# Optimization experiments

Measured on AMD Instinct MI355X. Metric: run time of the kernel, lower is better.

Reference implementation:

```python
import jax, jax.numpy as jnp
import numpy as np

NUM_HEADS = 8
BN_EPS = 1e-5
ATTN_EPS = 1e-6

def setup_inputs() -> dict:
    key = jax.random.key(0)
    N, E, D = 50000, 600000, 128
    ks = jax.random.split(key, 7)
    s = 1.0 / np.sqrt(D).astype(np.float32)
    return {
        'x': jax.random.normal(ks[0], (N, D), jnp.float32),
        'edge_attr': jax.random.normal(ks[1], (E, D), jnp.float32),
        'WQ': jax.random.normal(ks[2], (D, D), jnp.float32) * s,
        'WK': jax.random.normal(ks[3], (D, D), jnp.float32) * s,
        'WV': jax.random.normal(ks[4], (D, D), jnp.float32) * s,
        'WE': jax.random.normal(ks[5], (D, D), jnp.float32) * s,
        'bn_gamma': jnp.ones((D,), jnp.float32),
        'bn_beta': jnp.zeros((D,), jnp.float32),
        'edge_index': jax.random.randint(ks[6], (2, E), 0, N, dtype=jnp.int32),
    }

def reference(x, edge_attr, WQ, WK, WV, WE, bn_gamma, bn_beta, edge_index):
    N, D = x.shape
    H = NUM_HEADS
    dh = D // H  # head dim
    # Projections (no bias), split into heads: [N, H, dh]
    Q = (x @ WQ).reshape(N, H, dh)
    K = (x @ WK).reshape(N, H, dh)
    V = (x @ WV).reshape(N, H, dh)
    Eh = (edge_attr @ WE).reshape(-1, H, dh)  # [E, H, dh]
    src, dst = edge_index[0], edge_index[1]
    # Per-edge attention score modulated by edge features
    score = (K[src] * Q[dst]) / jnp.sqrt(jnp.float32(dh)) * Eh  # [E, H, dh]
    score = jnp.exp(jnp.clip(score.sum(-1, keepdims=True), -5.0, 5.0))  # [E, H, 1]
    msg = V[src] * score  # [E, H, dh]
    wV = jax.ops.segment_sum(msg, dst, num_segments=N)  # [N, H, dh]
    Z = jax.ops.segment_sum(score, dst, num_segments=N)  # [N, H, 1]
    h_attn = (wV / (Z + ATTN_EPS)).reshape(N, D)
    # Residual (dropout p=0 is identity) + BatchNorm1d (training statistics)
    h = x + h_attn
    mean = h.mean(axis=0)
    var = jnp.mean((h - mean) ** 2, axis=0)
    return (h - mean) * jax.lax.rsqrt(var + BN_EPS) * bn_gamma + bn_beta
```

## Files before the change

kernel.cpp:

```cpp
#include <hip/hip_runtime.h>
#include <math.h>


typedef __attribute__((ext_vector_type(8))) short short8;
typedef __attribute__((ext_vector_type(4))) float f32x4;

__device__ __forceinline__ unsigned short f2bf(float x) {
    unsigned int u = __float_as_uint(x);
    return (unsigned short)((u + 0x7FFFu + ((u >> 16) & 1u)) >> 16);
}

__global__ __launch_bounds__(128) void qkv_kernel(
    const float* __restrict__ x, const float* __restrict__ WQ,
    const float* __restrict__ WK, const float* __restrict__ WV,
    float* __restrict__ Q, float* __restrict__ K, float* __restrict__ V,
    int N)
{
    const int t = threadIdx.x;
    const int r0 = blockIdx.x * 8;
    __shared__ float xs[8][128];
#pragma unroll
    for (int r = 0; r < 8; ++r)
        xs[r][t] = (r0 + r < N) ? x[(size_t)(r0 + r) * 128 + t] : 0.f;
    __syncthreads();

    float aq[8] = {0}, ak[8] = {0}, av[8] = {0};
#pragma unroll 2
    for (int k4 = 0; k4 < 32; ++k4) {
        const float* wq = WQ + (size_t)(k4 * 4) * 128 + t;
        const float* wk = WK + (size_t)(k4 * 4) * 128 + t;
        const float* wv = WV + (size_t)(k4 * 4) * 128 + t;
        float q0 = wq[0], q1 = wq[128], q2 = wq[256], q3 = wq[384];
        float k0 = wk[0], k1 = wk[128], k2 = wk[256], k3 = wk[384];
        float v0 = wv[0], v1 = wv[128], v2 = wv[256], v3 = wv[384];
#pragma unroll
        for (int r = 0; r < 8; ++r) {
            float4 xv = *(const float4*)&xs[r][k4 * 4];
            aq[r] += xv.x * q0 + xv.y * q1 + xv.z * q2 + xv.w * q3;
            ak[r] += xv.x * k0 + xv.y * k1 + xv.z * k2 + xv.w * k3;
            av[r] += xv.x * v0 + xv.y * v1 + xv.z * v2 + xv.w * v3;
        }
    }
#pragma unroll
    for (int r = 0; r < 8; ++r) {
        if (r0 + r < N) {
            const size_t o = (size_t)(r0 + r) * 128 + t;
            Q[o] = aq[r]; K[o] = ak[r]; V[o] = av[r];
        }
    }
}

__global__ __launch_bounds__(256) void wet_kernel(
    const float* __restrict__ WE, unsigned short* __restrict__ WEt)
{
    const int i = blockIdx.x * 256 + threadIdx.x;
    const int n = i >> 7, k = i & 127;
    WEt[i] = f2bf(WE[k * 128 + n]);
}

#define ASTRIDE 136
#define ESTRIDE 132

__global__ __launch_bounds__(256, 4) void eh_score_kernel(
    const float* __restrict__ ea, const unsigned short* __restrict__ WEt,
    const float* __restrict__ Q, const float* __restrict__ K,
    const int* __restrict__ src, const int* __restrict__ dst,
    float* __restrict__ score, int E)
{
    union Sm {
        unsigned short A[64 * ASTRIDE];
        float eh[64 * ESTRIDE];
    };
    __shared__ Sm sm;
    __shared__ int ssrc[64], sdst[64];
    const int t = threadIdx.x;
    const long e0 = (long)blockIdx.x * 64;

#pragma unroll
    for (int kk = 0; kk < 8; ++kk) {
        const int f = t + kk * 256;
        const int row = f >> 5, c4 = (f & 31) * 4;
        float4 v = make_float4(0.f, 0.f, 0.f, 0.f);
        if (e0 + row < E) v = *(const float4*)&ea[(size_t)(e0 + row) * 128 + c4];
        unsigned long long pk =  (unsigned long long)f2bf(v.x)
                              | ((unsigned long long)f2bf(v.y) << 16)
                              | ((unsigned long long)f2bf(v.z) << 32)
                              | ((unsigned long long)f2bf(v.w) << 48);
        *(unsigned long long*)&sm.A[row * ASTRIDE + c4] = pk;
    }
    if (t < 64) {
        const long e = e0 + t;
        ssrc[t] = (e < E) ? src[e] : 0;
        sdst[t] = (e < E) ? dst[e] : 0;
    }
    __syncthreads();

    const int w = t >> 6, l = t & 63;
    const int rb = (w >> 1) * 32, cb = (w & 1) * 64;
    const int lr = l & 15, quad = l >> 4;

    f32x4 acc[2][4];
#pragma unroll
    for (int i = 0; i < 2; ++i)
#pragma unroll
        for (int j = 0; j < 4; ++j) acc[i][j] = (f32x4){0.f, 0.f, 0.f, 0.f};

#pragma unroll
    for (int kb = 0; kb < 4; ++kb) {
        const int k0 = kb * 32 + quad * 8;
        short8 a0 = *(const short8*)&sm.A[(rb + lr) * ASTRIDE + k0];
        short8 a1 = *(const short8*)&sm.A[(rb + 16 + lr) * ASTRIDE + k0];
        short8 b0 = *(const short8*)&WEt[(cb + lr) * 128 + k0];
        short8 b1 = *(const short8*)&WEt[(cb + 16 + lr) * 128 + k0];
        short8 b2 = *(const short8*)&WEt[(cb + 32 + lr) * 128 + k0];
        short8 b3 = *(const short8*)&WEt[(cb + 48 + lr) * 128 + k0];
        acc[0][0] = __builtin_amdgcn_mfma_f32_16x16x32_bf16(a0, b0, acc[0][0], 0, 0, 0);
        acc[0][1] = __builtin_amdgcn_mfma_f32_16x16x32_bf16(a0, b1, acc[0][1], 0, 0, 0);
        acc[0][2] = __builtin_amdgcn_mfma_f32_16x16x32_bf16(a0, b2, acc[0][2], 0, 0, 0);
        acc[0][3] = __builtin_amdgcn_mfma_f32_16x16x32_bf16(a0, b3, acc[0][3], 0, 0, 0);
        acc[1][0] = __builtin_amdgcn_mfma_f32_16x16x32_bf16(a1, b0, acc[1][0], 0, 0, 0);
        acc[1][1] = __builtin_amdgcn_mfma_f32_16x16x32_bf16(a1, b1, acc[1][1], 0, 0, 0);
        acc[1][2] = __builtin_amdgcn_mfma_f32_16x16x32_bf16(a1, b2, acc[1][2], 0, 0, 0);
        acc[1][3] = __builtin_amdgcn_mfma_f32_16x16x32_bf16(a1, b3, acc[1][3], 0, 0, 0);
    }
    __syncthreads();

#pragma unroll
    for (int mi = 0; mi < 2; ++mi)
#pragma unroll
        for (int ni = 0; ni < 4; ++ni)
#pragma unroll
            for (int r = 0; r < 4; ++r)
                sm.eh[(rb + mi * 16 + quad * 4 + r) * ESTRIDE + cb + ni * 16 + lr] =
                    acc[mi][ni][r];
    __syncthreads();

#pragma unroll
    for (int pp = 0; pp < 2; ++pp) {
        const int p = t + pp * 256;
        const int e = p >> 3, h = p & 7;
        const long ge = e0 + e;
        if (ge < E) {
            const float* kp = K + (size_t)ssrc[e] * 128 + h * 16;
            const float* qp = Q + (size_t)sdst[e] * 128 + h * 16;
            const float* ep = &sm.eh[e * ESTRIDE + h * 16];
            float s = 0.f;
#pragma unroll
            for (int j = 0; j < 4; ++j) {
                float4 kv = *(const float4*)&kp[j * 4];
                float4 qv = *(const float4*)&qp[j * 4];
                float4 ev = *(const float4*)&ep[j * 4];
                s += kv.x * qv.x * ev.x + kv.y * qv.y * ev.y +
                     kv.z * qv.z * ev.z + kv.w * qv.w * ev.w;
            }
            score[ge * 8 + h] = __expf(fminf(fmaxf(s * 0.25f, -5.f), 5.f));
        }
    }
}

__global__ __launch_bounds__(256) void hist_kernel(
    const int* __restrict__ dst, int* __restrict__ counts, int E)
{
    const int e = blockIdx.x * 256 + threadIdx.x;
    if (e < E) atomicAdd(&counts[dst[e]], 1);
}

__global__ __launch_bounds__(256) void scan_chunk_kernel(
    const int* __restrict__ in, int* __restrict__ excl,
    int* __restrict__ chunksums, int n)
{
    __shared__ int sm[256];
    const int t = threadIdx.x;
    const int i = blockIdx.x * 256 + t;
    const int v = (i < n) ? in[i] : 0;
    sm[t] = v;
    __syncthreads();
#pragma unroll
    for (int off = 1; off < 256; off <<= 1) {
        const int a = (t >= off) ? sm[t - off] : 0;
        __syncthreads();
        sm[t] += a;
        __syncthreads();
    }
    if (i < n) excl[i] = sm[t] - v;
    if (t == 255 && chunksums) chunksums[blockIdx.x] = sm[255];
}

__global__ __launch_bounds__(256) void add_offsets_kernel(
    int* __restrict__ excl, int* __restrict__ cursor,
    const int* __restrict__ chunkoff, int n)
{
    const int i = blockIdx.x * 256 + threadIdx.x;
    if (i < n) {
        const int v = excl[i] + chunkoff[blockIdx.x];
        excl[i] = v;
        cursor[i] = v;
    }
}

__global__ __launch_bounds__(256) void fill_perm_kernel(
    const int* __restrict__ dst, int* __restrict__ cursor,
    int* __restrict__ perm, int E)
{
    const int e = blockIdx.x * 256 + threadIdx.x;
    if (e < E) {
        const int slot = atomicAdd(&cursor[dst[e]], 1);
        perm[slot] = e;
    }
}

__global__ __launch_bounds__(256) void aggregate_kernel(
    const float* __restrict__ V, const float* __restrict__ score,
    const int* __restrict__ src, const int* __restrict__ perm,
    const int* __restrict__ seg_start, const int* __restrict__ counts,
    const float* __restrict__ x, float* __restrict__ out,
    float* __restrict__ sums, int N)
{
    const int t = threadIdx.x;
    const int w = t >> 6, lane = t & 63;
    const int ha = lane >> 4, hb = 4 + (lane >> 4);
    float s1a = 0.f, s1b = 0.f, s2a = 0.f, s2b = 0.f;

    for (int node = blockIdx.x * 4 + w; node < N; node += gridDim.x * 4) {
        const int beg = seg_start[node];
        const int cnt = counts[node];
        float acc0 = 0.f, acc1 = 0.f, za = 0.f, zb = 0.f;
        for (int j = 0; j < cnt; ++j) {
            const int e = perm[beg + j];
            const int s = src[e];
            const float sa = score[(size_t)e * 8 + ha];
            const float sb = score[(size_t)e * 8 + hb];
            acc0 += sa * V[(size_t)s * 128 + lane];
            acc1 += sb * V[(size_t)s * 128 + 64 + lane];
            za += sa; zb += sb;
        }
        const size_t o = (size_t)node * 128 + lane;
        const float hv0 = x[o] + acc0 / (za + 1e-6f);
        const float hv1 = x[o + 64] + acc1 / (zb + 1e-6f);
        out[o] = hv0;
        out[o + 64] = hv1;
        s1a += hv0; s1b += hv1;
        s2a += hv0 * hv0; s2b += hv1 * hv1;
    }

    __shared__ float red[4][128];
    red[w][lane] = s1a; red[w][lane + 64] = s1b;
    __syncthreads();
    if (t < 128) atomicAdd(&sums[t], red[0][t] + red[1][t] + red[2][t] + red[3][t]);
    __syncthreads();
    red[w][lane] = s2a; red[w][lane + 64] = s2b;
    __syncthreads();
    if (t < 128) atomicAdd(&sums[128 + t], red[0][t] + red[1][t] + red[2][t] + red[3][t]);
}

__global__ void bn_scale_kernel(
    const float* __restrict__ sums,
    const float* __restrict__ gamma, const float* __restrict__ beta,
    float* __restrict__ sb, int N)
{
    const int c = threadIdx.x;
    const float invN = 1.0f / (float)N;
    const float mean = sums[c] * invN;
    const float var = sums[128 + c] * invN - mean * mean;
    const float sc = gamma[c] * rsqrtf(var + 1e-5f);
    sb[c] = sc;
    sb[128 + c] = beta[c] - mean * sc;
}

__global__ __launch_bounds__(256) void bn_apply_kernel(
    float* hw, const float* __restrict__ sb, size_t total)
{
    __shared__ float ssb[256];
    ssb[threadIdx.x] = sb[threadIdx.x];
    __syncthreads();
    const size_t n4 = total / 4;
    float4* h4 = (float4*)hw;
    for (size_t i = (size_t)blockIdx.x * blockDim.x + threadIdx.x; i < n4;
         i += (size_t)gridDim.x * blockDim.x) {
        const int c4 = (int)(i & 31) * 4;
        float4 v = h4[i];
        v.x = v.x * ssb[c4 + 0] + ssb[128 + c4 + 0];
        v.y = v.y * ssb[c4 + 1] + ssb[128 + c4 + 1];
        v.z = v.z * ssb[c4 + 2] + ssb[128 + c4 + 2];
        v.w = v.w * ssb[c4 + 3] + ssb[128 + c4 + 3];
        h4[i] = v;
    }
}

extern "C" void kernel_launch(void* const* d_in, const int* in_sizes, int n_in,
                              void* d_out, int out_size, void* d_ws, size_t ws_size,
                              hipStream_t stream)
{
    const float* x         = (const float*)d_in[0];
    const float* edge_attr = (const float*)d_in[1];
    const float* WQ        = (const float*)d_in[2];
    const float* WK        = (const float*)d_in[3];
    const float* WV        = (const float*)d_in[4];
    const float* WE        = (const float*)d_in[5];
    const float* gamma     = (const float*)d_in[6];
    const float* beta      = (const float*)d_in[7];
    const int*   eidx      = (const int*)d_in[8];

    const int N = in_sizes[0] / 128;
    const int E = in_sizes[8] / 2;
    const int* src = eidx;
    const int* dst = eidx + E;

    float* ws = (float*)d_ws;
    const size_t NB = (size_t)N * 128;
    float* Q     = ws;
    float* K     = ws + NB;
    float* V     = ws + 2 * NB;
    float* score = ws + 3 * NB;
    float* sums  = score + (size_t)E * 8;
    float* sb    = sums + 256;
    unsigned short* WEt = (unsigned short*)(sb + 256);
    int* counts    = (int*)(WEt + 128 * 128);
    int* seg_start = counts + N;
    int* cursor    = seg_start + N;
    int* chunksums = cursor + N;
    int* chunkoff  = chunksums + 256;
    int* perm      = chunkoff + 256;
    float* out = (float*)d_out;

    const int nch = (N + 255) / 256;

    hipMemsetAsync(counts, 0, (size_t)N * sizeof(int), stream);
    hipMemsetAsync(sums, 0, 256 * sizeof(float), stream);

    qkv_kernel<<<(N + 7) / 8, 128, 0, stream>>>(x, WQ, WK, WV, Q, K, V, N);
    wet_kernel<<<64, 256, 0, stream>>>(WE, WEt);
    eh_score_kernel<<<(E + 63) / 64, 256, 0, stream>>>(edge_attr, WEt, Q, K, src, dst,
                                                       score, E);
    hist_kernel<<<(E + 255) / 256, 256, 0, stream>>>(dst, counts, E);
    scan_chunk_kernel<<<nch, 256, 0, stream>>>(counts, seg_start, chunksums, N);
    scan_chunk_kernel<<<1, 256, 0, stream>>>(chunksums, chunkoff, nullptr, nch);
    add_offsets_kernel<<<nch, 256, 0, stream>>>(seg_start, cursor, chunkoff, N);
    fill_perm_kernel<<<(E + 255) / 256, 256, 0, stream>>>(dst, cursor, perm, E);
    aggregate_kernel<<<3200, 256, 0, stream>>>(V, score, src, perm, seg_start, counts,
                                               x, out, sums, N);
    bn_scale_kernel<<<1, 128, 0, stream>>>(sums, gamma, beta, sb, N);
    bn_apply_kernel<<<2048, 256, 0, stream>>>(out, sb, NB);
}
```

Measured before the change: 856.4 us.

## Scatter scores into dst-sorted order and prefetch next edge in aggregation

The CSR build now runs before the score kernel, and each edge records its sorted slot. The score kernel writes its results straight into dst-sorted positions, and source indices are stored pre-permuted. Aggregation then reads scores and sources contiguously per node instead of chasing perm->src->score indirections. The aggregation loop also software-pipelines the loads for the next edge. In exchange, score writes become scattered and the fill kernel does an extra store.

```diff
diff --git a/kernel.cpp b/kernel.cpp
--- a/kernel.cpp
+++ b/kernel.cpp
@@ -65,6 +65,7 @@
     const float* __restrict__ ea, const unsigned short* __restrict__ WEt,
     const float* __restrict__ Q, const float* __restrict__ K,
     const int* __restrict__ src, const int* __restrict__ dst,
+    const int* __restrict__ eslot,
     float* __restrict__ score, int E)
 {
     union Sm {
@@ -72,7 +73,7 @@
         float eh[64 * ESTRIDE];
     };
     __shared__ Sm sm;
-    __shared__ int ssrc[64], sdst[64];
+    __shared__ int ssrc[64], sdst[64], sslot[64];
     const int t = threadIdx.x;
     const long e0 = (long)blockIdx.x * 64;
 
@@ -90,8 +91,9 @@
     }
     if (t < 64) {
         const long e = e0 + t;
-        ssrc[t] = (e < E) ? src[e] : 0;
-        sdst[t] = (e < E) ? dst[e] : 0;
+        ssrc[t]  = (e < E) ? src[e] : 0;
+        sdst[t]  = (e < E) ? dst[e] : 0;
+        sslot[t] = (e < E) ? eslot[e] : 0;
     }
     __syncthreads();
 
@@ -153,7 +155,7 @@
                 s += kv.x * qv.x * ev.x + kv.y * qv.y * ev.y +
                      kv.z * qv.z * ev.z + kv.w * qv.w * ev.w;
             }
-            score[ge * 8 + h] = __expf(fminf(fmaxf(s * 0.25f, -5.f), 5.f));
+            score[(size_t)sslot[e] * 8 + h] = __expf(fminf(fmaxf(s * 0.25f, -5.f), 5.f));
         }
     }
 }
@@ -198,20 +200,22 @@
     }
 }
 
-__global__ __launch_bounds__(256) void fill_perm_kernel(
-    const int* __restrict__ dst, int* __restrict__ cursor,
-    int* __restrict__ perm, int E)
+__global__ __launch_bounds__(256) void fill_sort_kernel(
+    const int* __restrict__ src, const int* __restrict__ dst,
+    int* __restrict__ cursor, int* __restrict__ eslot,
+    int* __restrict__ srcs, int E)
 {
     const int e = blockIdx.x * 256 + threadIdx.x;
     if (e < E) {
         const int slot = atomicAdd(&cursor[dst[e]], 1);
-        perm[slot] = e;
+        eslot[e] = slot;
+        srcs[slot] = src[e];
     }
 }
 
 __global__ __launch_bounds__(256) void aggregate_kernel(
     const float* __restrict__ V, const float* __restrict__ score,
-    const int* __restrict__ src, const int* __restrict__ perm,
+    const int* __restrict__ srcs,
     const int* __restrict__ seg_start, const int* __restrict__ counts,
     const float* __restrict__ x, float* __restrict__ out,
     float* __restrict__ sums, int N)
@@ -225,14 +229,24 @@
         const int beg = seg_start[node];
         const int cnt = counts[node];
         float acc0 = 0.f, acc1 = 0.f, za = 0.f, zb = 0.f;
-        for (int j = 0; j < cnt; ++j) {
-            const int e = perm[beg + j];
-            const int s = src[e];
-            const float sa = score[(size_t)e * 8 + ha];
-            const float sb = score[(size_t)e * 8 + hb];
-            acc0 += sa * V[(size_t)s * 128 + lane];
-            acc1 += sb * V[(size_t)s * 128 + 64 + lane];
-            za += sa; zb += sb;
+        if (cnt > 0) {
+            int sA = srcs[beg];
+            float saA = score[(size_t)beg * 8 + ha];
+            float sbA = score[(size_t)beg * 8 + hb];
+            const float* vA = V + (size_t)sA * 128;
+            float vA0 = vA[lane], vA1 = vA[lane + 64];
+            for (int j = 1; j < cnt; ++j) {
+                const int sB = srcs[beg + j];
+                const float saB = score[(size_t)(beg + j) * 8 + ha];
+                const float sbB = score[(size_t)(beg + j) * 8 + hb];
+                const float* vB = V + (size_t)sB * 128;
+                const float vB0 = vB[lane], vB1 = vB[lane + 64];
+                acc0 += saA * vA0; za += saA;
+                acc1 += sbA * vA1; zb += sbA;
+                saA = saB; sbA = sbB; vA0 = vB0; vA1 = vB1;
+            }
+            acc0 += saA * vA0; za += saA;
+            acc1 += sbA * vA1; zb += sbA;
         }
         const size_t o = (size_t)node * 128 + lane;
         const float hv0 = x[o] + acc0 / (za + 1e-6f);
@@ -320,7 +334,8 @@
     int* cursor    = seg_start + N;
     int* chunksums = cursor + N;
     int* chunkoff  = chunksums + 256;
-    int* perm      = chunkoff + 256;
+    int* eslot     = chunkoff + 256;
+    int* srcs      = eslot + E;
     float* out = (float*)d_out;
 
     const int nch = (N + 255) / 256;
@@ -330,14 +345,15 @@
 
     qkv_kernel<<<(N + 7) / 8, 128, 0, stream>>>(x, WQ, WK, WV, Q, K, V, N);
     wet_kernel<<<64, 256, 0, stream>>>(WE, WEt);
-    eh_score_kernel<<<(E + 63) / 64, 256, 0, stream>>>(edge_attr, WEt, Q, K, src, dst,
-                                                       score, E);
     hist_kernel<<<(E + 255) / 256, 256, 0, stream>>>(dst, counts, E);
     scan_chunk_kernel<<<nch, 256, 0, stream>>>(counts, seg_start, chunksums, N);
     scan_chunk_kernel<<<1, 256, 0, stream>>>(chunksums, chunkoff, nullptr, nch);
     add_offsets_kernel<<<nch, 256, 0, stream>>>(seg_start, cursor, chunkoff, N);
-    fill_perm_kernel<<<(E + 255) / 256, 256, 0, stream>>>(dst, cursor, perm, E);
-    aggregate_kernel<<<3200, 256, 0, stream>>>(V, score, src, perm, seg_start, counts,
+    fill_sort_kernel<<<(E + 255) / 256, 256, 0, stream>>>(src, dst, cursor, eslot,
+                                                          srcs, E);
+    eh_score_kernel<<<(E + 63) / 64, 256, 0, stream>>>(edge_attr, WEt, Q, K, src, dst,
+                                                       eslot, score, E);
+    aggregate_kernel<<<3200, 256, 0, stream>>>(V, score, srcs, seg_start, counts,
                                                x, out, sums, N);
     bn_scale_kernel<<<1, 128, 0, stream>>>(sums, gamma, beta, sb, N);
     bn_apply_kernel<<<2048, 256, 0, stream>>>(out, sb, NB);
```

New measurement: 851.1 us. No clear change (-0.6%).
